# Performance work log

Hardware: AMD Instinct MI355X
Metric: run time of the kernel (lower is better)

The kernel has to match this reference:

```python
import jax, jax.numpy as jnp
import numpy as np

B, T, D, H = 2, 2048, 1024, 16
NEG = -65504.0


def setup_inputs() -> dict:
    key = jax.random.key(0)
    ks = jax.random.split(key, 12)
    std = float(np.sqrt(2.0 / (D + D)))  # xavier_normal for square weights
    inp = {
        'q': jax.random.normal(ks[0], (B, T, D), jnp.float32),
        'k': jax.random.normal(ks[1], (B, T, D), jnp.float32),
        'v': jax.random.normal(ks[2], (B, T, D), jnp.float32),
        'mask': jax.random.randint(ks[3], (B, T), 0, 2, jnp.int32),
        # weights stored as (in, out) so y = x @ W + b
        'Wq': jax.random.normal(ks[4], (D, D), jnp.float32) * std,
        'bq': jnp.zeros((D,), jnp.float32),
        'Wk': jax.random.normal(ks[5], (D, D), jnp.float32) * std,
        'bk': jnp.zeros((D,), jnp.float32),
        'Wv': jax.random.normal(ks[6], (D, D), jnp.float32) * std,
        'bv': jnp.zeros((D,), jnp.float32),
        'Wo': jax.random.normal(ks[7], (D, D), jnp.float32) * std,
        'bo': jnp.zeros((D,), jnp.float32),
    }
    return inp


def reference(q, k, v, mask, Wq, bq, Wk, bk, Wv, bv, Wo, bo):
    b, t, _ = q.shape
    dim_a = Wq.shape[1]
    dh = dim_a // H
    # projections, then split into heads: (b, t, H, dh)
    qh = (q @ Wq + bq).reshape(b, t, H, dh)
    kh = (k @ Wk + bk).reshape(b, t, H, dh)
    vh = (v @ Wv + bv).reshape(b, t, H, dh)
    # NOTE: module scales by 1/sqrt(dim_a) with the FULL dim_a, not per-head
    a = jnp.einsum('bthd,bshd->bhts', qh, kh) / jnp.sqrt(jnp.float32(dim_a))
    # 2D mask broadcasts over query positions: (b, 1, 1, t_keys)
    a = jnp.where(mask[:, None, None, :] == 0, NEG, a)
    a = jax.nn.softmax(a, axis=-1)  # dropout_prob=0 (eval mode)
    o = jnp.einsum('bhts,bshd->bthd', a, vh).reshape(b, t, dim_a)
    return o @ Wo + bo
```

## Files before the change

### kernel.cpp

```cpp
#include <hip/hip_runtime.h>
#include <hip/hip_bf16.h>
#include <math.h>

#define B_ 2
#define T_ 2048
#define D_ 1024
#define H_ 16
#define QSCALE (0.03125f * 1.44269504088896f)

typedef _Float16 f16;
using f16x4 = __attribute__((ext_vector_type(4))) _Float16;
using f16x8 = __attribute__((ext_vector_type(8))) _Float16;
using f32x4 = __attribute__((ext_vector_type(4))) float;

__device__ __forceinline__ void gl16(const void* g, void* l) {
  __builtin_amdgcn_global_load_lds(
      (__attribute__((address_space(1))) void*)g,
      (__attribute__((address_space(3))) void*)l, 16, 0, 0);
}

__global__ __launch_bounds__(256) void prep(
    const int* __restrict__ mask,
    const float* __restrict__ Wq, const float* __restrict__ Wk,
    const float* __restrict__ Wv, const float* __restrict__ Wo,
    const float* __restrict__ bq, const float* __restrict__ bk,
    const float* __restrict__ bv, const float* __restrict__ bo,
    f16* __restrict__ Wt, float* __restrict__ bias,
    int* __restrict__ idx, int* __restrict__ inv, int* __restrict__ nk,
    f16* __restrict__ khc) {
  __shared__ float sh[64][65];
  const int bid = blockIdx.x;
  const int tid = threadIdx.x;

  if (bid < 1024) {
    const int z = bid >> 8;
    const int k0 = ((bid >> 4) & 15) * 64, n0 = (bid & 15) * 64;
    const float* W = (z == 0) ? Wq : (z == 1) ? Wk : (z == 2) ? Wv : Wo;
    const int r = tid >> 2, c0 = (tid & 3) * 16;
#pragma unroll
    for (int i = 0; i < 4; ++i)
      *(float4*)&sh[r][c0 + 4 * i] =
          *(const float4*)&W[(size_t)(k0 + r) * 1024 + n0 + c0 + 4 * i];
    __syncthreads();
    f16 tmp[16];
#pragma unroll
    for (int i = 0; i < 16; ++i) tmp[i] = (f16)sh[c0 + i][r];
    f16* dst = Wt + (size_t)z * 1048576 + (size_t)(n0 + r) * 1024 + k0 + c0;
    *(f16x8*)dst = *(f16x8*)&tmp[0];
    *(f16x8*)(dst + 8) = *(f16x8*)&tmp[8];
  } else if (bid < 1040) {
    const int i = (bid - 1024) * 256 + tid;
    const int z = i >> 10;
    const float* s = (z == 0) ? bq : (z == 1) ? bk : (z == 2) ? bv : bo;
    bias[i] = s[i & 1023];
  } else {
    const int b = bid - 1040;
    int* cnt = (int*)sh;
    int loc[8];
    int c = 0;
#pragma unroll
    for (int i = 0; i < 8; ++i) {
      loc[i] = mask[b * T_ + tid * 8 + i];
      c += loc[i];
    }
    cnt[tid] = c;
    __syncthreads();
    for (int off = 1; off < 256; off <<= 1) {
      int vsh = (tid >= off) ? cnt[tid - off] : 0;
      __syncthreads();
      cnt[tid] += vsh;
      __syncthreads();
    }
    int pos = cnt[tid] - c;
#pragma unroll
    for (int i = 0; i < 8; ++i) {
      const int t = tid * 8 + i;
      if (loc[i]) {
        idx[b * T_ + pos] = t;
        inv[b * T_ + t] = pos;
        ++pos;
      } else {
        inv[b * T_ + t] = -1;
      }
    }
    const int n = cnt[255];
    if (tid == 255) nk[b] = n;
    const int nkt = (n + 63) >> 6;
    const int npadrows = (nkt << 6) - n;
    uint4 z4 = {0u, 0u, 0u, 0u};
    f16* base = khc + ((size_t)b * T_ + n) * D_;
    for (int i = tid; i < npadrows * 128; i += 256)
      *(uint4*)(base + (size_t)i * 8) = z4;
  }
}

__global__ __launch_bounds__(256) void gemm_qkv(
    const float* __restrict__ xq, const float* __restrict__ xk,
    const float* __restrict__ xv, const f16* __restrict__ Wtb,
    const float* __restrict__ biasb, f16* __restrict__ qh,
    f16* __restrict__ khc, f16* __restrict__ vh,
    const int* __restrict__ inv) {
  __shared__ __align__(16) f16 As[128 * 32];
  __shared__ __align__(16) f16 Bs[128 * 32];
  const int z = blockIdx.z;
  const float* X = (z == 0) ? xq : (z == 1) ? xk : xv;
  const f16* Wt = Wtb + (size_t)z * 1048576;
  const float* bias = biasb + (size_t)z * 1024;
  f16* C = (z == 0) ? qh : (z == 1) ? khc : vh;

  const int tid = threadIdx.x;
  const int wave = tid >> 6, lane = tid & 63;
  const int quad = lane >> 4, l16 = lane & 15;
  const int wm = wave & 1, wn = wave >> 1;
  const int m0 = blockIdx.y * 128, n0 = blockIdx.x * 128;

  f32x4 acc[4][4] = {};

  const float* asrc = X + (size_t)(m0 + (tid >> 2)) * 1024 + (tid & 3) * 8;
  const f16* bsrc = Wt + (size_t)(n0 + (tid >> 2)) * 1024 + (tid & 3) * 8;
  char* bldst = (char*)Bs + tid * 16;
  f16* aw0 = As + tid * 8;
  f16* aw1 = As + 2048 + tid * 8;

  float ar[16];
  auto loadA = [&](int k0) {
    float4 x0 = *(const float4*)(asrc + k0);
    float4 x1 = *(const float4*)(asrc + k0 + 4);
    float4 x2 = *(const float4*)(asrc + 65536 + k0);
    float4 x3 = *(const float4*)(asrc + 65536 + k0 + 4);
    ar[0] = x0.x; ar[1] = x0.y; ar[2] = x0.z; ar[3] = x0.w;
    ar[4] = x1.x; ar[5] = x1.y; ar[6] = x1.z; ar[7] = x1.w;
    ar[8] = x2.x; ar[9] = x2.y; ar[10] = x2.z; ar[11] = x2.w;
    ar[12] = x3.x; ar[13] = x3.y; ar[14] = x3.z; ar[15] = x3.w;
  };
  loadA(0);

  for (int kt = 0; kt < 32; ++kt) {
    if (kt) __syncthreads();
    gl16(bsrc, bldst);
    gl16(bsrc + 65536, bldst + 4096);
    bsrc += 32;
    f16x8 h0, h1;
#pragma unroll
    for (int i = 0; i < 8; ++i) { h0[i] = (f16)ar[i]; h1[i] = (f16)ar[8 + i]; }
    *(f16x8*)aw0 = h0;
    *(f16x8*)aw1 = h1;
    __syncthreads();
    if (kt + 1 < 32) loadA(32 * (kt + 1));

    f16x8 af[4], bf[4];
#pragma unroll
    for (int t = 0; t < 4; ++t)
      af[t] = *(const f16x8*)&As[(64 * wm + 16 * t + l16) * 32 + quad * 8];
#pragma unroll
    for (int t = 0; t < 4; ++t)
      bf[t] = *(const f16x8*)&Bs[(64 * wn + 16 * t + l16) * 32 + quad * 8];
#pragma unroll
    for (int i = 0; i < 4; ++i)
#pragma unroll
      for (int j = 0; j < 4; ++j)
        acc[i][j] = __builtin_amdgcn_mfma_f32_16x16x32_f16(af[i], bf[j], acc[i][j], 0, 0, 0);
  }

  const int cm = m0 + 64 * wm + 4 * quad;
  const int cn = n0 + 64 * wn + l16;
  float bv[4];
#pragma unroll
  for (int tn = 0; tn < 4; ++tn) bv[tn] = bias[cn + 16 * tn];

  if (z == 1) {
    const int bb = m0 >> 11;
#pragma unroll
    for (int tm = 0; tm < 4; ++tm) {
#pragma unroll
      for (int r = 0; r < 4; ++r) {
        const int m = cm + 16 * tm + r;
        const int j = inv[m];
        if (j >= 0) {
          f16* row = C + ((size_t)(bb << 11) + j) * 1024;
#pragma unroll
          for (int tn = 0; tn < 4; ++tn)
            row[cn + 16 * tn] = (f16)(acc[tm][tn][r] + bv[tn]);
        }
      }
    }
  } else {
    const float scl = (z == 0) ? QSCALE : 1.f;
#pragma unroll
    for (int tm = 0; tm < 4; ++tm)
#pragma unroll
      for (int r = 0; r < 4; ++r) {
        f16* row = C + (size_t)(cm + 16 * tm + r) * 1024;
#pragma unroll
        for (int tn = 0; tn < 4; ++tn)
          row[cn + 16 * tn] = (f16)((acc[tm][tn][r] + bv[tn]) * scl);
      }
  }
}

__global__ __launch_bounds__(256) void vtrans(
    const f16* __restrict__ vh, const int* __restrict__ idx,
    const int* __restrict__ nk, f16* __restrict__ vhT) {
  const int tt = blockIdx.x, bh = blockIdx.y;
  const int b = bh >> 4, h = bh & 15;
  const int n = nk[b];
  const int nkt = (n + 63) >> 6;
  if (tt >= nkt) return;
  __shared__ f16 t[64][72];
  const int tid = threadIdx.x;
  const int r = tid >> 2, cq = 16 * (tid & 3);

  const int j = tt * 64 + r;
  uint4 v0 = {0u, 0u, 0u, 0u}, v1 = {0u, 0u, 0u, 0u};
  if (j < n) {
    const int tsrc = idx[b * T_ + j];
    const uint4* src = (const uint4*)(vh + ((size_t)b * T_ + tsrc) * D_ + h * 64 + cq);
    v0 = src[0]; v1 = src[1];
  }
  *(uint4*)&t[r][cq]     = v0;
  *(uint4*)&t[r][cq + 8] = v1;
  __syncthreads();

  f16 tmp[16];
#pragma unroll
  for (int xx = 0; xx < 16; ++xx) {
    int x = (xx + r) & 15;
    tmp[x] = t[cq + x][r];
  }
  f16* dst = vhT + ((size_t)bh * 64 + r) * T_ + tt * 64 + cq;
  *(uint4*)&dst[0] = *(uint4*)&tmp[0];
  *(uint4*)&dst[8] = *(uint4*)&tmp[8];
}

__global__ __launch_bounds__(256) void attn_mfma(
    const f16* __restrict__ qh, const f16* __restrict__ khc,
    const f16* __restrict__ vhT, const int* __restrict__ nkd,
    f16* __restrict__ opart, float* __restrict__ lpart) {
  __shared__ f16 Ks[64][72];
  __shared__ f16 Vt[64][72];
  __shared__ f16 Ps[4][32][72];

  const int qt = blockIdx.x, bh = blockIdx.y, ks = blockIdx.z;
  const int b = bh >> 4, h = bh & 15;
  const int tid = threadIdx.x;
  const int wave = tid >> 6, lane = tid & 63;
  const int quad = lane >> 4, l16 = lane & 15;
  const int sr = tid >> 2, sq = 16 * (tid & 3);

  const int n = nkd[b];
  const int nkt = (n + 63) >> 6;
  const int hn = (nkt + 1) >> 1;
  const int t_begin = ks ? hn : 0;
  const int t_end = ks ? nkt : hn;
  const bool owns_last = (t_end == nkt) && (t_end > t_begin);
  const int npad = (nkt << 6) - n;

  f16x8 qf[2][2];
#pragma unroll
  for (int gq = 0; gq < 2; ++gq) {
    const f16* qp = qh + ((size_t)(b * T_ + qt * 128 + wave * 32 + 16 * gq + l16)) * D_ + h * 64 + quad * 8;
    qf[gq][0] = *(const f16x8*)qp;
    qf[gq][1] = *(const f16x8*)(qp + 32);
  }

  float lsum[2] = {0.f, 0.f};
  f32x4 o[2][4] = {};

  const f16* kbase = khc + (size_t)b * T_ * D_ + h * 64;
  const f16* vbase = vhT + ((size_t)bh * 64 + sr) * T_;

  uint4 kr0, kr1, vr0, vr1;
  auto load_kv = [&](int kt) {
    const uint4* kp = (const uint4*)(kbase + (size_t)(kt * 64 + sr) * D_ + sq);
    kr0 = kp[0]; kr1 = kp[1];
    const uint4* vp = (const uint4*)(vbase + kt * 64 + sq);
    vr0 = vp[0]; vr1 = vp[1];
  };
  if (t_begin < t_end) load_kv(t_begin);

  for (int kt = t_begin; kt < t_end; ++kt) {
    *(uint4*)&Ks[sr][sq]     = kr0;
    *(uint4*)&Ks[sr][sq + 8] = kr1;
    *(uint4*)&Vt[sr][sq]     = vr0;
    *(uint4*)&Vt[sr][sq + 8] = vr1;
    __syncthreads();
    if (kt + 1 < t_end) load_kv(kt + 1);

#pragma unroll
    for (int tn = 0; tn < 4; ++tn) {
      f16x8 kf0 = *(const f16x8*)&Ks[16 * tn + l16][quad * 8];
      f16x8 kf1 = *(const f16x8*)&Ks[16 * tn + l16][32 + quad * 8];
#pragma unroll
      for (int gq = 0; gq < 2; ++gq) {
        f32x4 s = {0.f, 0.f, 0.f, 0.f};
        s = __builtin_amdgcn_mfma_f32_16x16x32_f16(kf0, qf[gq][0], s, 0, 0, 0);
        s = __builtin_amdgcn_mfma_f32_16x16x32_f16(kf1, qf[gq][1], s, 0, 0, 0);
        float p0 = exp2f(s[0]), p1 = exp2f(s[1]);
        float p2 = exp2f(s[2]), p3 = exp2f(s[3]);
        lsum[gq] += (p0 + p1) + (p2 + p3);
        f16x4 pk;
        pk[0] = (f16)p0; pk[1] = (f16)p1; pk[2] = (f16)p2; pk[3] = (f16)p3;
        *(f16x4*)&Ps[wave][16 * gq + l16][16 * tn + 4 * quad] = pk;
      }
    }

    f16x8 pf[2][2];
#pragma unroll
    for (int gq = 0; gq < 2; ++gq) {
      pf[gq][0] = *(const f16x8*)&Ps[wave][16 * gq + l16][quad * 8];
      pf[gq][1] = *(const f16x8*)&Ps[wave][16 * gq + l16][32 + quad * 8];
    }
#pragma unroll
    for (int t = 0; t < 4; ++t) {
      f16x8 vf0 = *(const f16x8*)&Vt[16 * t + l16][quad * 8];
      f16x8 vf1 = *(const f16x8*)&Vt[16 * t + l16][32 + quad * 8];
#pragma unroll
      for (int gq = 0; gq < 2; ++gq) {
        o[gq][t] = __builtin_amdgcn_mfma_f32_16x16x32_f16(pf[gq][0], vf0, o[gq][t], 0, 0, 0);
        o[gq][t] = __builtin_amdgcn_mfma_f32_16x16x32_f16(pf[gq][1], vf1, o[gq][t], 0, 0, 0);
      }
    }
    __syncthreads();
  }

  f16* obase = opart + (size_t)ks * 4194304;
  float* lbase = lpart + (size_t)ks * 65536 + (size_t)bh * 2048;
#pragma unroll
  for (int gq = 0; gq < 2; ++gq) {
    float ls = lsum[gq];
    ls += __shfl_xor(ls, 16);
    ls += __shfl_xor(ls, 32);
    if (owns_last) ls -= (float)npad;
    const int qrow0 = qt * 128 + wave * 32 + 16 * gq;
    if (quad == 0) lbase[qrow0 + l16] = ls;
    const size_t orow = (size_t)(b * T_ + qrow0 + 4 * quad);
#pragma unroll
    for (int r = 0; r < 4; ++r)
#pragma unroll
      for (int t = 0; t < 4; ++t)
        obase[(orow + r) * D_ + h * 64 + 16 * t + l16] = (f16)o[gq][t][r];
  }
}

__global__ __launch_bounds__(256) void gemm_out(
    const f16* __restrict__ opart, const float* __restrict__ lpart,
    const f16* __restrict__ Wt3, const float* __restrict__ bias3,
    float* __restrict__ out) {
  __shared__ __align__(16) f16 As[64 * 32];
  __shared__ __align__(16) f16 Bs[128 * 32];
  const int tid = threadIdx.x;
  const int wave = tid >> 6, lane = tid & 63;
  const int quad = lane >> 4, l16 = lane & 15;
  const int wm = wave & 1, wn = wave >> 1;
  const int m0 = blockIdx.y * 64, n0 = blockIdx.x * 128;

  f32x4 acc[2][4] = {};

  const int row = m0 + (tid >> 2);
  const int cq = (tid & 3) * 8;
  const f16* oa = opart + (size_t)row * 1024 + cq;
  const f16* ob = oa + 4194304;
  const float* lp = lpart + (size_t)(row >> 11) * 32768 + (row & 2047);
  const f16* bsrc = Wt3 + (size_t)(n0 + (tid >> 2)) * 1024 + cq;
  char* bldst = (char*)Bs + tid * 16;

  for (int kt = 0; kt < 32; ++kt) {
    if (kt) __syncthreads();
    gl16(bsrc, bldst);
    gl16(bsrc + 65536, bldst + 4096);
    bsrc += 32;
    const int h = (kt * 32 + cq) >> 6;
    const float la = lp[h * 2048];
    const float lb = lp[65536 + h * 2048];
    const float invl = 1.f / (la + lb);
    f16x8 a8 = *(const f16x8*)(oa + kt * 32);
    f16x8 b8 = *(const f16x8*)(ob + kt * 32);
    f16x8 hv;
#pragma unroll
    for (int i = 0; i < 8; ++i)
      hv[i] = (f16)(((float)a8[i] + (float)b8[i]) * invl);
    *(f16x8*)(As + tid * 8) = hv;
    __syncthreads();

    f16x8 af[2], bf[4];
#pragma unroll
    for (int t = 0; t < 2; ++t)
      af[t] = *(const f16x8*)&As[(32 * wm + 16 * t + l16) * 32 + quad * 8];
#pragma unroll
    for (int t = 0; t < 4; ++t)
      bf[t] = *(const f16x8*)&Bs[(64 * wn + 16 * t + l16) * 32 + quad * 8];
#pragma unroll
    for (int i = 0; i < 2; ++i)
#pragma unroll
      for (int j = 0; j < 4; ++j)
        acc[i][j] = __builtin_amdgcn_mfma_f32_16x16x32_f16(af[i], bf[j], acc[i][j], 0, 0, 0);
  }

  const int cm = m0 + 32 * wm + 4 * quad;
  const int cn = n0 + 64 * wn + l16;
#pragma unroll
  for (int tn = 0; tn < 4; ++tn) {
    const float bv = bias3[cn + 16 * tn];
#pragma unroll
    for (int tm = 0; tm < 2; ++tm)
#pragma unroll
      for (int r = 0; r < 4; ++r)
        out[(size_t)(cm + 16 * tm + r) * 1024 + cn + 16 * tn] = acc[tm][tn][r] + bv;
  }
}

extern "C" void kernel_launch(void* const* d_in, const int* in_sizes, int n_in,
                              void* d_out, int out_size, void* d_ws, size_t ws_size,
                              hipStream_t stream) {
  const float* q  = (const float*)d_in[0];
  const float* k  = (const float*)d_in[1];
  const float* v  = (const float*)d_in[2];
  const int* mask = (const int*)d_in[3];
  const float* Wq = (const float*)d_in[4];
  const float* bq = (const float*)d_in[5];
  const float* Wk = (const float*)d_in[6];
  const float* bk = (const float*)d_in[7];
  const float* Wv = (const float*)d_in[8];
  const float* bv = (const float*)d_in[9];
  const float* Wo = (const float*)d_in[10];
  const float* bo = (const float*)d_in[11];
  float* out = (float*)d_out;

  char* ws = (char*)d_ws;
  f16* qh     = (f16*)(ws);
  f16* vh     = (f16*)(ws + 8388608);
  f16* khc    = (f16*)(ws + 16777216);
  f16* vhT    = (f16*)(ws + 25165824);
  f16* opart  = (f16*)(ws + 33554432);
  f16* Wt     = (f16*)(ws + 50331648);
  float* lpart = (float*)(ws + 58720256);
  float* bsw  = (float*)(ws + 59244544);
  int* idx    = (int*)(ws + 59260928);
  int* inv    = (int*)(ws + 59277312);
  int* nk     = (int*)(ws + 59293696);

  dim3 blk(256);

  prep<<<dim3(1042), blk, 0, stream>>>(mask, Wq, Wk, Wv, Wo, bq, bk, bv, bo,
                                       Wt, bsw, idx, inv, nk, khc);

  gemm_qkv<<<dim3(8, 32, 3), blk, 0, stream>>>(q, k, v, Wt, bsw,
                                               qh, khc, vh, inv);

  vtrans<<<dim3(32, 32), blk, 0, stream>>>(vh, idx, nk, vhT);

  attn_mfma<<<dim3(16, 32, 2), blk, 0, stream>>>(qh, khc, vhT, nk,
                                                 opart, lpart);

  gemm_out<<<dim3(8, 64), blk, 0, stream>>>(opart, lpart, Wt + 3145728,
                                            bsw + 3072, out);
}
```

Before: 246.7 us.

## Pre-convert activations to fp16 in prep and load GEMM A tiles via direct-to-LDS

Adds a pass in the prep kernel that converts the q/k/v fp32 activations to fp16 into a workspace buffer. The QKV GEMM then loads A tiles with global_load_lds like the B tiles, dropping the register staging and in-loop fp32-to-fp16 conversion. This halves the bytes the GEMM reads for A, at the cost of an extra full read/write pass over the activations in prep. The workspace layout is reshuffled so vhT/opart alias the now-dead xqkv region.

Result: faster. 230.4 us (-6.6%).

```diff
diff --git a/kernel.cpp b/kernel.cpp
--- a/kernel.cpp
+++ b/kernel.cpp
@@ -20,21 +20,33 @@
 }
 
 __global__ __launch_bounds__(256) void prep(
-    const int* __restrict__ mask,
+    const float* __restrict__ q, const float* __restrict__ k,
+    const float* __restrict__ v, const int* __restrict__ mask,
     const float* __restrict__ Wq, const float* __restrict__ Wk,
     const float* __restrict__ Wv, const float* __restrict__ Wo,
     const float* __restrict__ bq, const float* __restrict__ bk,
     const float* __restrict__ bv, const float* __restrict__ bo,
-    f16* __restrict__ Wt, float* __restrict__ bias,
+    f16* __restrict__ xqkv, f16* __restrict__ Wt, float* __restrict__ bias,
     int* __restrict__ idx, int* __restrict__ inv, int* __restrict__ nk,
     f16* __restrict__ khc) {
   __shared__ float sh[64][65];
   const int bid = blockIdx.x;
   const int tid = threadIdx.x;
 
-  if (bid < 1024) {
-    const int z = bid >> 8;
-    const int k0 = ((bid >> 4) & 15) * 64, n0 = (bid & 15) * 64;
+  if (bid < 6144) {
+    const int z = bid / 2048;
+    const float* src = (z == 0) ? q : (z == 1) ? k : v;
+    const size_t i = ((size_t)(bid % 2048) * 256 + tid) * 8;
+    float4 a = *(const float4*)(src + i);
+    float4 b = *(const float4*)(src + i + 4);
+    f16x8 o;
+    o[0] = (f16)a.x; o[1] = (f16)a.y; o[2] = (f16)a.z; o[3] = (f16)a.w;
+    o[4] = (f16)b.x; o[5] = (f16)b.y; o[6] = (f16)b.z; o[7] = (f16)b.w;
+    *(f16x8*)(xqkv + (size_t)z * 4194304 + i) = o;
+  } else if (bid < 7168) {
+    const int id = bid - 6144;
+    const int z = id >> 8;
+    const int k0 = ((id >> 4) & 15) * 64, n0 = (id & 15) * 64;
     const float* W = (z == 0) ? Wq : (z == 1) ? Wk : (z == 2) ? Wv : Wo;
     const int r = tid >> 2, c0 = (tid & 3) * 16;
 #pragma unroll
@@ -48,13 +60,13 @@
     f16* dst = Wt + (size_t)z * 1048576 + (size_t)(n0 + r) * 1024 + k0 + c0;
     *(f16x8*)dst = *(f16x8*)&tmp[0];
     *(f16x8*)(dst + 8) = *(f16x8*)&tmp[8];
-  } else if (bid < 1040) {
-    const int i = (bid - 1024) * 256 + tid;
+  } else if (bid < 7184) {
+    const int i = (bid - 7168) * 256 + tid;
     const int z = i >> 10;
     const float* s = (z == 0) ? bq : (z == 1) ? bk : (z == 2) ? bv : bo;
     bias[i] = s[i & 1023];
   } else {
-    const int b = bid - 1040;
+    const int b = bid - 7184;
     int* cnt = (int*)sh;
     int loc[8];
     int c = 0;
@@ -95,15 +107,14 @@
 }
 
 __global__ __launch_bounds__(256) void gemm_qkv(
-    const float* __restrict__ xq, const float* __restrict__ xk,
-    const float* __restrict__ xv, const f16* __restrict__ Wtb,
+    const f16* __restrict__ Xb, const f16* __restrict__ Wtb,
     const float* __restrict__ biasb, f16* __restrict__ qh,
     f16* __restrict__ khc, f16* __restrict__ vh,
     const int* __restrict__ inv) {
   __shared__ __align__(16) f16 As[128 * 32];
   __shared__ __align__(16) f16 Bs[128 * 32];
   const int z = blockIdx.z;
-  const float* X = (z == 0) ? xq : (z == 1) ? xk : xv;
+  const f16* X = Xb + (size_t)z * 4194304;
   const f16* Wt = Wtb + (size_t)z * 1048576;
   const float* bias = biasb + (size_t)z * 1024;
   f16* C = (z == 0) ? qh : (z == 1) ? khc : vh;
@@ -116,37 +127,19 @@
 
   f32x4 acc[4][4] = {};
 
-  const float* asrc = X + (size_t)(m0 + (tid >> 2)) * 1024 + (tid & 3) * 8;
+  const f16* asrc = X + (size_t)(m0 + (tid >> 2)) * 1024 + (tid & 3) * 8;
   const f16* bsrc = Wt + (size_t)(n0 + (tid >> 2)) * 1024 + (tid & 3) * 8;
+  char* aldst = (char*)As + tid * 16;
   char* bldst = (char*)Bs + tid * 16;
-  f16* aw0 = As + tid * 8;
-  f16* aw1 = As + 2048 + tid * 8;
-
-  float ar[16];
-  auto loadA = [&](int k0) {
-    float4 x0 = *(const float4*)(asrc + k0);
-    float4 x1 = *(const float4*)(asrc + k0 + 4);
-    float4 x2 = *(const float4*)(asrc + 65536 + k0);
-    float4 x3 = *(const float4*)(asrc + 65536 + k0 + 4);
-    ar[0] = x0.x; ar[1] = x0.y; ar[2] = x0.z; ar[3] = x0.w;
-    ar[4] = x1.x; ar[5] = x1.y; ar[6] = x1.z; ar[7] = x1.w;
-    ar[8] = x2.x; ar[9] = x2.y; ar[10] = x2.z; ar[11] = x2.w;
-    ar[12] = x3.x; ar[13] = x3.y; ar[14] = x3.z; ar[15] = x3.w;
-  };
-  loadA(0);
 
   for (int kt = 0; kt < 32; ++kt) {
     if (kt) __syncthreads();
+    gl16(asrc, aldst);
+    gl16(asrc + 65536, aldst + 4096);
     gl16(bsrc, bldst);
     gl16(bsrc + 65536, bldst + 4096);
-    bsrc += 32;
-    f16x8 h0, h1;
-#pragma unroll
-    for (int i = 0; i < 8; ++i) { h0[i] = (f16)ar[i]; h1[i] = (f16)ar[8 + i]; }
-    *(f16x8*)aw0 = h0;
-    *(f16x8*)aw1 = h1;
-    __syncthreads();
-    if (kt + 1 < 32) loadA(32 * (kt + 1));
+    asrc += 32; bsrc += 32;
+    __syncthreads();
 
     f16x8 af[4], bf[4];
 #pragma unroll
@@ -427,24 +420,26 @@
   float* out = (float*)d_out;
 
   char* ws = (char*)d_ws;
-  f16* qh     = (f16*)(ws);
-  f16* vh     = (f16*)(ws + 8388608);
-  f16* khc    = (f16*)(ws + 16777216);
-  f16* vhT    = (f16*)(ws + 25165824);
-  f16* opart  = (f16*)(ws + 33554432);
-  f16* Wt     = (f16*)(ws + 50331648);
+  f16* xqkv   = (f16*)(ws);
+  f16* Wt     = (f16*)(ws + 25165824);
+  f16* qh     = (f16*)(ws + 33554432);
+  f16* vh     = (f16*)(ws + 41943040);
+  f16* khc    = (f16*)(ws + 50331648);
   float* lpart = (float*)(ws + 58720256);
   float* bsw  = (float*)(ws + 59244544);
   int* idx    = (int*)(ws + 59260928);
   int* inv    = (int*)(ws + 59277312);
   int* nk     = (int*)(ws + 59293696);
+  f16* vhT    = (f16*)(ws);
+  f16* opart  = (f16*)(ws + 8388608);
 
   dim3 blk(256);
 
-  prep<<<dim3(1042), blk, 0, stream>>>(mask, Wq, Wk, Wv, Wo, bq, bk, bv, bo,
-                                       Wt, bsw, idx, inv, nk, khc);
-
-  gemm_qkv<<<dim3(8, 32, 3), blk, 0, stream>>>(q, k, v, Wt, bsw,
+  prep<<<dim3(7186), blk, 0, stream>>>(q, k, v, mask, Wq, Wk, Wv, Wo,
+                                       bq, bk, bv, bo, xqkv, Wt, bsw,
+                                       idx, inv, nk, khc);
+
+  gemm_qkv<<<dim3(8, 32, 3), blk, 0, stream>>>(xqkv, Wt, bsw,
                                                qh, khc, vh, inv);
 
   vtrans<<<dim3(32, 32), blk, 0, stream>>>(vh, idx, nk, vhT);
```
